# Kernel tuning notes

Hardware: AMD Instinct MI355X
Metric: run time of the kernel (lower is better)

## Reference

```python
import jax, jax.numpy as jnp
import numpy as np

N = 100000      # nodes
E = 1600000     # edges (avg degree 16)
IN, HID, OUT = 64, 64, 32
R = 8           # relations


def setup_inputs() -> dict:
    key = jax.random.key(0)
    ks = jax.random.split(key, 8)
    s = jnp.float32(0.05)  # weight init scale
    return {
        "feat": jax.random.normal(ks[0], (N, IN), dtype=jnp.float32),
        "src": jax.random.randint(ks[1], (E,), 0, N),
        "dst": jax.random.randint(ks[2], (E,), 0, N),
        "etypes": jax.random.randint(ks[3], (E,), 0, R),
        "W1": jax.random.normal(ks[4], (R, IN, HID), dtype=jnp.float32) * s,
        "Wself1": jax.random.normal(ks[5], (IN, HID), dtype=jnp.float32) * s,
        "b1": jnp.zeros((HID,), jnp.float32),
        "W2": jax.random.normal(ks[6], (R, HID, OUT), dtype=jnp.float32) * s,
        "Wself2": jax.random.normal(ks[7], (HID, OUT), dtype=jnp.float32) * s,
        "b2": jnp.zeros((OUT,), jnp.float32),
    }


def _rel_graph_conv(h, src, dst, etypes, W, Wself, b):
    """RelGraphConv with sum aggregation, self-loop and bias.

    h: [N, din], W: [R, din, dout], Wself: [din, dout], b: [dout].
    """
    n = h.shape[0]
    # Transform all nodes by all relation weights once: [R, N, dout].
    hW = jnp.einsum('nd,rdo->rno', h, W)
    # Per-edge message: relation-specific transform of the source node.
    msg = hW[etypes, src]                                    # [E, dout]
    # Scatter-add messages to destination nodes.
    agg = jax.ops.segment_sum(msg, dst, num_segments=n)      # [N, dout]
    return agg + h @ Wself + b


def reference(feat, src, dst, etypes, W1, Wself1, b1, W2, Wself2, b2):
    x = jax.nn.relu(_rel_graph_conv(feat, src, dst, etypes, W1, Wself1, b1))
    return _rel_graph_conv(x, src, dst, etypes, W2, Wself2, b2)
```

## Files before the change

kernel.cpp:

```cpp
#include <hip/hip_runtime.h>
#include <hip/hip_bf16.h>

typedef __attribute__((ext_vector_type(8))) short short8;
typedef __attribute__((ext_vector_type(4))) float f32x4;

__device__ __forceinline__ unsigned short f2bf(float v) {
    __hip_bfloat16 h = __float2bfloat16(v);
    return *reinterpret_cast<unsigned short*>(&h);
}
__device__ __forceinline__ float bf2f(unsigned short u) {
    union { unsigned int i; float f; } x;
    x.i = (unsigned int)u << 16;
    return x.f;
}
__device__ __forceinline__ void acc4(float& s0, float& s1, float& s2, float& s3, uint2 v) {
    s0 += bf2f((unsigned short)(v.x & 0xffff));
    s1 += bf2f((unsigned short)(v.x >> 16));
    s2 += bf2f((unsigned short)(v.y & 0xffff));
    s3 += bf2f((unsigned short)(v.y >> 16));
}

__device__ __forceinline__ void lds_barrier() {
    asm volatile("s_waitcnt lgkmcnt(0)" ::: "memory");
    __builtin_amdgcn_s_barrier();
    asm volatile("" ::: "memory");
}

constexpr int MAXB  = 2048;
constexpr int MAXPB = 1792;

template<int H>
__global__ __launch_bounds__(256) void transpose_w(
    const float* __restrict__ W, const float* __restrict__ Wself,
    unsigned short* __restrict__ Wt, int R)
{
    int i = blockIdx.x * 256 + threadIdx.x;
    int total = (R + 1) * H * 64;
    if (i >= total) return;
    int d = i & 63;
    int hh = i >> 6;
    int r = hh / H, h = hh % H;
    float v = (r < R) ? W[((size_t)r * 64 + d) * H + h]
                      : Wself[(size_t)d * H + h];
    Wt[i] = f2bf(v);
}

template<int H, int RT, bool ABF, bool SBF>
__global__ __launch_bounds__(512) void gemm_rel_mfma(
    const void* __restrict__ Av, const unsigned short* __restrict__ Wt,
    const float* __restrict__ bias,
    unsigned short* __restrict__ C, void* __restrict__ Cselfv,
    int N, int Rrt, int relu)
{
    constexpr int AS = 72;
    constexpr int CPB = (H == 64) ? 72 : 40;
    __shared__ unsigned short As[64 * AS];
    alignas(16) __shared__ float Csf[2][64 * 36];
    const int R = RT ? RT : Rrt;
    const int tid = threadIdx.x;
    const int n0 = blockIdx.x * 64;

    if constexpr (ABF) {
        const unsigned short* A = (const unsigned short*)Av;
        int n = tid >> 3, d8 = (tid & 7) * 8;
        int gn = n0 + n;
        short8 u = {};
        if (gn < N) u = *(const short8*)&A[(size_t)gn * 64 + d8];
        if (relu) {
            #pragma unroll
            for (int j = 0; j < 8; ++j) {
                unsigned short x = (unsigned short)u[j];
                u[j] = (short)((x & 0x8000) ? 0 : x);
            }
        }
        *(short8*)&As[n * AS + d8] = u;
    } else {
        const float* A = (const float*)Av;
        #pragma unroll
        for (int i = 0; i < 2; ++i) {
            int lin = tid + i * 512;
            int n = lin >> 4;
            int d4 = (lin & 15) * 4;
            int gn = n0 + n;
            float4 v = make_float4(0.f, 0.f, 0.f, 0.f);
            if (gn < N) v = *(const float4*)&A[(size_t)gn * 64 + d4];
            if (relu) {
                v.x = fmaxf(v.x, 0.f); v.y = fmaxf(v.y, 0.f);
                v.z = fmaxf(v.z, 0.f); v.w = fmaxf(v.w, 0.f);
            }
            ushort4 u;
            u.x = f2bf(v.x); u.y = f2bf(v.y); u.z = f2bf(v.z); u.w = f2bf(v.w);
            *(ushort4*)&As[n * AS + d4] = u;
        }
    }

    const int w = tid >> 6, lane = tid & 63;
    const int m = lane & 15, quad = lane >> 4;
    const int wt = w & 3;
    const int half = w >> 2;

    lds_barrier();

    short8 afrag[2];
    afrag[0] = *(const short8*)&As[(wt * 16 + m) * AS + 0 * 32 + quad * 8];
    afrag[1] = *(const short8*)&As[(wt * 16 + m) * AS + 1 * 32 + quad * 8];

    constexpr int NT = H / 32;

    auto wptr = [&](int r, int nt, int kc) {
        int colbase = half * (H / 2) + nt * 16;
        return (const short8*)&Wt[((size_t)(r * H + colbase + m)) * 64 + kc * 32 + quad * 8];
    };

    short8 wf0[NT][2], wf1[NT][2];
    #pragma unroll
    for (int nt = 0; nt < NT; ++nt) { wf0[nt][0] = *wptr(0, nt, 0); wf0[nt][1] = *wptr(0, nt, 1); }
    #pragma unroll
    for (int nt = 0; nt < NT; ++nt) { wf1[nt][0] = *wptr(1, nt, 0); wf1[nt][1] = *wptr(1, nt, 1); }

    #pragma unroll
    for (int r = 0; r <= R; ++r) {
        short8 wn[NT][2];
        if (r + 2 <= R) {
            #pragma unroll
            for (int nt = 0; nt < NT; ++nt) {
                wn[nt][0] = *wptr(r + 2, nt, 0);
                wn[nt][1] = *wptr(r + 2, nt, 1);
            }
        }

        f32x4 acc[NT];
        #pragma unroll
        for (int nt = 0; nt < NT; ++nt) {
            acc[nt] = (f32x4){0.f, 0.f, 0.f, 0.f};
            acc[nt] = __builtin_amdgcn_mfma_f32_16x16x32_bf16(wf0[nt][0], afrag[0], acc[nt], 0, 0, 0);
            acc[nt] = __builtin_amdgcn_mfma_f32_16x16x32_bf16(wf0[nt][1], afrag[1], acc[nt], 0, 0, 0);
        }

        unsigned short* Cb = (unsigned short*)Csf[r & 1];
        float* Cf = Csf[r & 1];
        if (r < R) {
            #pragma unroll
            for (int nt = 0; nt < NT; ++nt) {
                int col = half * (H / 2) + nt * 16 + quad * 4;
                ushort4 u;
                u.x = f2bf(acc[nt][0]); u.y = f2bf(acc[nt][1]);
                u.z = f2bf(acc[nt][2]); u.w = f2bf(acc[nt][3]);
                *(ushort4*)&Cb[(wt * 16 + m) * CPB + col] = u;
            }
        } else if constexpr (SBF) {
            #pragma unroll
            for (int nt = 0; nt < NT; ++nt) {
                int col = half * (H / 2) + nt * 16 + quad * 4;
                const float4 bv = *(const float4*)&bias[col];
                ushort4 u;
                u.x = f2bf(acc[nt][0] + bv.x); u.y = f2bf(acc[nt][1] + bv.y);
                u.z = f2bf(acc[nt][2] + bv.z); u.w = f2bf(acc[nt][3] + bv.w);
                *(ushort4*)&Cb[(wt * 16 + m) * CPB + col] = u;
            }
        } else {
            #pragma unroll
            for (int nt = 0; nt < NT; ++nt) {
                int col = half * (H / 2) + nt * 16 + quad * 4;
                const float4 bv = *(const float4*)&bias[col];
                float4 o = make_float4(acc[nt][0] + bv.x, acc[nt][1] + bv.y,
                                       acc[nt][2] + bv.z, acc[nt][3] + bv.w);
                *(float4*)&Cf[(wt * 16 + m) * 36 + col] = o;
            }
        }

        lds_barrier();

        if (r < R) {
            if (H == 64) {
                int rw = tid >> 3, ch = tid & 7;
                int gn = n0 + rw;
                if (gn < N) {
                    uint4 v = *(const uint4*)&Cb[rw * CPB + ch * 8];
                    *(uint4*)&C[((size_t)r * N + gn) * H + ch * 8] = v;
                }
            } else {
                if (tid < 256) {
                    int rw = tid >> 2, ch = tid & 3;
                    int gn = n0 + rw;
                    if (gn < N) {
                        uint4 v = *(const uint4*)&Cb[rw * CPB + ch * 8];
                        *(uint4*)&C[((size_t)r * N + gn) * H + ch * 8] = v;
                    }
                }
            }
        } else if constexpr (SBF) {
            unsigned short* Cs = (unsigned short*)Cselfv;
            int rw = tid >> 3, ch = tid & 7;
            int gn = n0 + rw;
            if (gn < N) {
                uint4 v = *(const uint4*)&Cb[rw * CPB + ch * 8];
                *(uint4*)&Cs[(size_t)gn * H + ch * 8] = v;
            }
        } else {
            float* outf = (float*)Cselfv;
            int rw = tid >> 3, ch = tid & 7;
            int gn = n0 + rw;
            if (gn < N) {
                float4 v = *(const float4*)&Cf[rw * 36 + ch * 4];
                *(float4*)&outf[(size_t)gn * 32 + ch * 4] = v;
            }
        }

        #pragma unroll
        for (int nt = 0; nt < NT; ++nt) {
            wf0[nt][0] = wf1[nt][0]; wf0[nt][1] = wf1[nt][1];
            wf1[nt][0] = wn[nt][0];  wf1[nt][1] = wn[nt][1];
        }
    }
}

__global__ __launch_bounds__(256) void zero_int(int* __restrict__ p, int n) {
    int i = blockIdx.x * 256 + threadIdx.x;
    if (i < n) p[i] = 0;
}

__global__ __launch_bounds__(256) void partition_pad(
    const int* __restrict__ src, const int* __restrict__ dst,
    const int* __restrict__ et, int* __restrict__ gcnt,
    int* __restrict__ rec, int E, int N, int B, int CH)
{
    __shared__ int cnt[MAXB];
    __shared__ int base[MAXB];
    const int t = threadIdx.x;
    const int e0 = blockIdx.x * CH, e1 = min(E, e0 + CH);

    for (int i = t; i < B; i += 256) cnt[i] = 0;
    __syncthreads();
    for (int e = e0 + t; e < e1; e += 256) atomicAdd(&cnt[dst[e] >> 6], 1);
    __syncthreads();
    for (int i = t; i < B; i += 256) {
        int h = cnt[i];
        base[i] = h ? atomicAdd(&gcnt[i], h) : 0;
        cnt[i] = 0;
    }
    __syncthreads();
    for (int e = e0 + t; e < e1; e += 256) {
        int d = dst[e];
        int b = d >> 6;
        int pos = base[b] + atomicAdd(&cnt[b], 1);
        if (pos < MAXPB)
            rec[(size_t)b * MAXPB + pos] = ((et[e] * N + src[e]) << 6) | (d & 63);
    }
}

__global__ __launch_bounds__(256) void bucket_sort(
    const int* __restrict__ gcnt, const int* __restrict__ rec,
    int* __restrict__ eidx, int* __restrict__ rs, int* __restrict__ re_,
    int N)
{
    __shared__ int hist[64];
    __shared__ int excl[64];
    __shared__ int cur[64];
    const int b = blockIdx.x;
    const int tid = threadIdx.x;
    const int p0 = b * MAXPB;
    const int ne = min(gcnt[b], MAXPB);

    if (tid < 64) hist[tid] = 0;
    __syncthreads();
    for (int p = tid; p < ne; p += 256)
        atomicAdd(&hist[rec[p0 + p] & 63], 1);
    __syncthreads();
    if (tid == 0) {
        int run = 0;
        #pragma unroll
        for (int i = 0; i < 64; ++i) { excl[i] = run; run += hist[i]; }
    }
    __syncthreads();
    if (tid < 64) {
        cur[tid] = excl[tid];
        int n = b * 64 + tid;
        if (n < N) {
            rs[n]  = p0 + excl[tid];
            re_[n] = p0 + excl[tid] + hist[tid];
        }
    }
    __syncthreads();
    for (int p = tid; p < ne; p += 256) {
        int rv = rec[p0 + p];
        int pos = p0 + atomicAdd(&cur[rv & 63], 1);
        eidx[pos] = rv >> 6;
    }
}

__global__ __launch_bounds__(256) void agg_csr64(
    const unsigned int* __restrict__ hw32, const int* __restrict__ rs,
    const int* __restrict__ re_, const int* __restrict__ eidx,
    unsigned int* __restrict__ out32, int N)
{
    const int d = blockIdx.x * 4 + (threadIdx.x >> 6);
    const int lane = threadIdx.x & 63;
    if (d >= N) return;
    const int g = lane >> 4;
    const int c = lane & 15;
    const int p0 = rs[d], p1 = re_[d];
    float s0 = 0.f, s1 = 0.f, s2 = 0.f, s3 = 0.f;
    int p = p0 + g;
    for (; p + 12 < p1; p += 16) {
        uint2 v0 = *(const uint2*)&hw32[(size_t)eidx[p]      * 32 + 2 * c];
        uint2 v1 = *(const uint2*)&hw32[(size_t)eidx[p + 4]  * 32 + 2 * c];
        uint2 v2 = *(const uint2*)&hw32[(size_t)eidx[p + 8]  * 32 + 2 * c];
        uint2 v3 = *(const uint2*)&hw32[(size_t)eidx[p + 12] * 32 + 2 * c];
        acc4(s0, s1, s2, s3, v0);
        acc4(s0, s1, s2, s3, v1);
        acc4(s0, s1, s2, s3, v2);
        acc4(s0, s1, s2, s3, v3);
    }
    for (; p < p1; p += 4) {
        uint2 v = *(const uint2*)&hw32[(size_t)eidx[p] * 32 + 2 * c];
        acc4(s0, s1, s2, s3, v);
    }
    s0 += __shfl_xor(s0, 16, 64); s1 += __shfl_xor(s1, 16, 64);
    s2 += __shfl_xor(s2, 16, 64); s3 += __shfl_xor(s3, 16, 64);
    s0 += __shfl_xor(s0, 32, 64); s1 += __shfl_xor(s1, 32, 64);
    s2 += __shfl_xor(s2, 32, 64); s3 += __shfl_xor(s3, 32, 64);
    if (g == 0) {
        uint2 cur = *(const uint2*)&out32[(size_t)d * 32 + 2 * c];
        float o0 = s0 + bf2f((unsigned short)(cur.x & 0xffff));
        float o1 = s1 + bf2f((unsigned short)(cur.x >> 16));
        float o2 = s2 + bf2f((unsigned short)(cur.y & 0xffff));
        float o3 = s3 + bf2f((unsigned short)(cur.y >> 16));
        uint2 o;
        o.x = (unsigned int)f2bf(o0) | ((unsigned int)f2bf(o1) << 16);
        o.y = (unsigned int)f2bf(o2) | ((unsigned int)f2bf(o3) << 16);
        *(uint2*)&out32[(size_t)d * 32 + 2 * c] = o;
    }
}

__global__ __launch_bounds__(256) void agg_csr32(
    const unsigned int* __restrict__ hw32, const int* __restrict__ rs,
    const int* __restrict__ re_, const int* __restrict__ eidx,
    float* __restrict__ out, int N)
{
    const int d = blockIdx.x * 8 + (threadIdx.x >> 5);
    const int l = threadIdx.x & 31;
    if (d >= N) return;
    const int g = l >> 3;
    const int c = l & 7;
    const int p0 = rs[d], p1 = re_[d];
    float s0 = 0.f, s1 = 0.f, s2 = 0.f, s3 = 0.f;
    int p = p0 + g;
    for (; p + 12 < p1; p += 16) {
        uint2 v0 = *(const uint2*)&hw32[(size_t)eidx[p]      * 16 + 2 * c];
        uint2 v1 = *(const uint2*)&hw32[(size_t)eidx[p + 4]  * 16 + 2 * c];
        uint2 v2 = *(const uint2*)&hw32[(size_t)eidx[p + 8]  * 16 + 2 * c];
        uint2 v3 = *(const uint2*)&hw32[(size_t)eidx[p + 12] * 16 + 2 * c];
        acc4(s0, s1, s2, s3, v0);
        acc4(s0, s1, s2, s3, v1);
        acc4(s0, s1, s2, s3, v2);
        acc4(s0, s1, s2, s3, v3);
    }
    for (; p < p1; p += 4) {
        uint2 v = *(const uint2*)&hw32[(size_t)eidx[p] * 16 + 2 * c];
        acc4(s0, s1, s2, s3, v);
    }
    s0 += __shfl_xor(s0, 8, 64);  s1 += __shfl_xor(s1, 8, 64);
    s2 += __shfl_xor(s2, 8, 64);  s3 += __shfl_xor(s3, 8, 64);
    s0 += __shfl_xor(s0, 16, 64); s1 += __shfl_xor(s1, 16, 64);
    s2 += __shfl_xor(s2, 16, 64); s3 += __shfl_xor(s3, 16, 64);
    if (g == 0) {
        float4 cur = *(const float4*)&out[(size_t)d * 32 + 4 * c];
        float4 o = make_float4(cur.x + s0, cur.y + s1, cur.z + s2, cur.w + s3);
        *(float4*)&out[(size_t)d * 32 + 4 * c] = o;
    }
}

extern "C" void kernel_launch(void* const* d_in, const int* in_sizes, int n_in,
                              void* d_out, int out_size, void* d_ws, size_t ws_size,
                              hipStream_t stream)
{
    const float* feat = (const float*)d_in[0];
    const int*   src  = (const int*)d_in[1];
    const int*   dst  = (const int*)d_in[2];
    const int*   et   = (const int*)d_in[3];
    const float* W1   = (const float*)d_in[4];
    const float* Ws1  = (const float*)d_in[5];
    const float* b1   = (const float*)d_in[6];
    const float* W2   = (const float*)d_in[7];
    const float* Ws2  = (const float*)d_in[8];
    const float* b2   = (const float*)d_in[9];
    float* out = (float*)d_out;

    const int N = in_sizes[0] / 64;
    const int E = in_sizes[1];
    const int R = in_sizes[4] / (64 * 64);
    const int B = (N + 63) / 64;

    unsigned short* hW  = (unsigned short*)d_ws;
    unsigned short* h1  = hW + (size_t)R * N * 64;
    unsigned short* Wt1 = h1 + (size_t)N * 64;
    unsigned short* Wt2 = Wt1 + (size_t)(R + 1) * 64 * 64;
    int*   gcnt  = (int*)(Wt2 + (size_t)(R + 1) * 32 * 64);
    int*   rs    = gcnt + B;
    int*   re_   = rs + N;
    int*   rec   = re_ + N;
    int*   eidx  = rec + (size_t)B * MAXPB;

    const dim3 blk(256);
    const int nblk64 = (N + 63) / 64;
    const int P  = 512;
    const int CH = (E + P - 1) / P;

    transpose_w<64><<<((R + 1) * 64 * 64 + 255) / 256, blk, 0, stream>>>(W1, Ws1, Wt1, R);
    transpose_w<32><<<((R + 1) * 32 * 64 + 255) / 256, blk, 0, stream>>>(W2, Ws2, Wt2, R);

    zero_int<<<(B + 255) / 256, blk, 0, stream>>>(gcnt, B);
    partition_pad<<<P, blk, 0, stream>>>(src, dst, et, gcnt, rec, E, N, B, CH);
    bucket_sort<<<B, blk, 0, stream>>>(gcnt, rec, eidx, rs, re_, N);

    if (R == 8)
        gemm_rel_mfma<64, 8, false, true><<<nblk64, 512, 0, stream>>>(feat, Wt1, b1, hW, h1, N, R, 0);
    else
        gemm_rel_mfma<64, 0, false, true><<<nblk64, 512, 0, stream>>>(feat, Wt1, b1, hW, h1, N, R, 0);
    agg_csr64<<<dim3((N + 3) / 4), blk, 0, stream>>>((const unsigned int*)hW, rs, re_, eidx,
                                                     (unsigned int*)h1, N);

    if (R == 8)
        gemm_rel_mfma<32, 8, true, false><<<nblk64, 512, 0, stream>>>(h1, Wt2, b2, hW, out, N, R, 1);
    else
        gemm_rel_mfma<32, 0, true, false><<<nblk64, 512, 0, stream>>>(h1, Wt2, b2, hW, out, N, R, 1);
    agg_csr32<<<dim3((N + 7) / 8), blk, 0, stream>>>((const unsigned int*)hW, rs, re_, eidx, out, N);
}
```

Measured before the change: 337.2 us.

## Fuse edge partition with layer-1 GEMM in one launch and merge weight transposes

```diff
diff --git a/kernel.cpp b/kernel.cpp
--- a/kernel.cpp
+++ b/kernel.cpp
@@ -28,37 +28,73 @@
 
 constexpr int MAXB  = 2048;
 constexpr int MAXPB = 1792;
-
-template<int H>
-__global__ __launch_bounds__(256) void transpose_w(
-    const float* __restrict__ W, const float* __restrict__ Wself,
-    unsigned short* __restrict__ Wt, int R)
+constexpr int SMEM  = 64 * 72 * 2 + 2 * 64 * 36 * 4;
+
+__global__ __launch_bounds__(256) void transpose_both(
+    const float* __restrict__ W1, const float* __restrict__ Ws1,
+    const float* __restrict__ W2, const float* __restrict__ Ws2,
+    unsigned short* __restrict__ Wt1, unsigned short* __restrict__ Wt2, int R)
 {
     int i = blockIdx.x * 256 + threadIdx.x;
-    int total = (R + 1) * H * 64;
-    if (i >= total) return;
-    int d = i & 63;
-    int hh = i >> 6;
-    int r = hh / H, h = hh % H;
-    float v = (r < R) ? W[((size_t)r * 64 + d) * H + h]
-                      : Wself[(size_t)d * H + h];
-    Wt[i] = f2bf(v);
+    int t1 = (R + 1) * 64 * 64;
+    int t2 = (R + 1) * 32 * 64;
+    if (i < t1) {
+        int d = i & 63, hh = i >> 6;
+        int r = hh >> 6, h = hh & 63;
+        float v = (r < R) ? W1[((size_t)r * 64 + d) * 64 + h] : Ws1[(size_t)d * 64 + h];
+        Wt1[i] = f2bf(v);
+    } else if (i < t1 + t2) {
+        int j = i - t1;
+        int d = j & 63, hh = j >> 6;
+        int r = hh >> 5, h = hh & 31;
+        float v = (r < R) ? W2[((size_t)r * 64 + d) * 32 + h] : Ws2[(size_t)d * 32 + h];
+        Wt2[j] = f2bf(v);
+    }
+}
+
+__device__ __forceinline__ void partition_body(
+    char* smem, const int* __restrict__ src, const int* __restrict__ dst,
+    const int* __restrict__ et, int* __restrict__ gcnt,
+    int* __restrict__ rec, int E, int N, int B, int CH, int bidx)
+{
+    int* cnt  = (int*)smem;
+    int* base = (int*)(smem + sizeof(int) * MAXB);
+    const int t = threadIdx.x;
+    const int e0 = bidx * CH, e1 = min(E, e0 + CH);
+
+    for (int i = t; i < B; i += 512) cnt[i] = 0;
+    __syncthreads();
+    for (int e = e0 + t; e < e1; e += 512) atomicAdd(&cnt[dst[e] >> 6], 1);
+    __syncthreads();
+    for (int i = t; i < B; i += 512) {
+        int h = cnt[i];
+        base[i] = h ? atomicAdd(&gcnt[i], h) : 0;
+        cnt[i] = 0;
+    }
+    __syncthreads();
+    for (int e = e0 + t; e < e1; e += 512) {
+        int d = dst[e];
+        int b = d >> 6;
+        int pos = base[b] + atomicAdd(&cnt[b], 1);
+        if (pos < MAXPB)
+            rec[(size_t)b * MAXPB + pos] = ((et[e] * N + src[e]) << 6) | (d & 63);
+    }
 }
 
 template<int H, int RT, bool ABF, bool SBF>
-__global__ __launch_bounds__(512) void gemm_rel_mfma(
-    const void* __restrict__ Av, const unsigned short* __restrict__ Wt,
+__device__ __forceinline__ void gemm_body(
+    char* smem, const void* __restrict__ Av, const unsigned short* __restrict__ Wt,
     const float* __restrict__ bias,
     unsigned short* __restrict__ C, void* __restrict__ Cselfv,
-    int N, int Rrt, int relu)
+    int N, int Rrt, int relu, int bidx)
 {
     constexpr int AS = 72;
     constexpr int CPB = (H == 64) ? 72 : 40;
-    __shared__ unsigned short As[64 * AS];
-    alignas(16) __shared__ float Csf[2][64 * 36];
+    unsigned short* As = (unsigned short*)smem;
+    float* CsfBase = (float*)(smem + 64 * AS * 2);
     const int R = RT ? RT : Rrt;
     const int tid = threadIdx.x;
-    const int n0 = blockIdx.x * 64;
+    const int n0 = bidx * 64;
 
     if constexpr (ABF) {
         const unsigned short* A = (const unsigned short*)Av;
@@ -137,8 +173,8 @@
             acc[nt] = __builtin_amdgcn_mfma_f32_16x16x32_bf16(wf0[nt][1], afrag[1], acc[nt], 0, 0, 0);
         }
 
-        unsigned short* Cb = (unsigned short*)Csf[r & 1];
-        float* Cf = Csf[r & 1];
+        float* Cf = CsfBase + (r & 1) * (64 * 36);
+        unsigned short* Cb = (unsigned short*)Cf;
         if (r < R) {
             #pragma unroll
             for (int nt = 0; nt < NT; ++nt) {
@@ -215,38 +251,33 @@
     }
 }
 
-__global__ __launch_bounds__(256) void zero_int(int* __restrict__ p, int n) {
-    int i = blockIdx.x * 256 + threadIdx.x;
-    if (i < n) p[i] = 0;
-}
-
-__global__ __launch_bounds__(256) void partition_pad(
+template<int RT>
+__global__ __launch_bounds__(512) void mega64(
+    const float* __restrict__ feat, const unsigned short* __restrict__ Wt1,
+    const float* __restrict__ b1, unsigned short* __restrict__ hW,
+    unsigned short* __restrict__ h1,
     const int* __restrict__ src, const int* __restrict__ dst,
-    const int* __restrict__ et, int* __restrict__ gcnt,
-    int* __restrict__ rec, int E, int N, int B, int CH)
-{
-    __shared__ int cnt[MAXB];
-    __shared__ int base[MAXB];
-    const int t = threadIdx.x;
-    const int e0 = blockIdx.x * CH, e1 = min(E, e0 + CH);
-
-    for (int i = t; i < B; i += 256) cnt[i] = 0;
-    __syncthreads();
-    for (int e = e0 + t; e < e1; e += 256) atomicAdd(&cnt[dst[e] >> 6], 1);
-    __syncthreads();
-    for (int i = t; i < B; i += 256) {
-        int h = cnt[i];
-        base[i] = h ? atomicAdd(&gcnt[i], h) : 0;
-        cnt[i] = 0;
-    }
-    __syncthreads();
-    for (int e = e0 + t; e < e1; e += 256) {
-        int d = dst[e];
-        int b = d >> 6;
-        int pos = base[b] + atomicAdd(&cnt[b], 1);
-        if (pos < MAXPB)
-            rec[(size_t)b * MAXPB + pos] = ((et[e] * N + src[e]) << 6) | (d & 63);
-    }
+    const int* __restrict__ et, int* __restrict__ gcnt, int* __restrict__ rec,
+    int E, int N, int B, int CH, int P, int R)
+{
+    __shared__ alignas(16) char smem[SMEM];
+    if ((int)blockIdx.x < P) {
+        partition_body(smem, src, dst, et, gcnt, rec, E, N, B, CH, blockIdx.x);
+    } else {
+        gemm_body<64, RT, false, true>(smem, feat, Wt1, b1, hW, h1, N, R, 0,
+                                       blockIdx.x - P);
+    }
+}
+
+template<int H, int RT, bool ABF, bool SBF>
+__global__ __launch_bounds__(512) void gemm_rel_mfma(
+    const void* __restrict__ Av, const unsigned short* __restrict__ Wt,
+    const float* __restrict__ bias,
+    unsigned short* __restrict__ C, void* __restrict__ Cselfv,
+    int N, int Rrt, int relu)
+{
+    __shared__ alignas(16) char smem[SMEM];
+    gemm_body<H, RT, ABF, SBF>(smem, Av, Wt, bias, C, Cselfv, N, Rrt, relu, blockIdx.x);
 }
 
 __global__ __launch_bounds__(256) void bucket_sort(
@@ -407,17 +438,23 @@
     const int P  = 512;
     const int CH = (E + P - 1) / P;
 
-    transpose_w<64><<<((R + 1) * 64 * 64 + 255) / 256, blk, 0, stream>>>(W1, Ws1, Wt1, R);
-    transpose_w<32><<<((R + 1) * 32 * 64 + 255) / 256, blk, 0, stream>>>(W2, Ws2, Wt2, R);
-
-    zero_int<<<(B + 255) / 256, blk, 0, stream>>>(gcnt, B);
-    partition_pad<<<P, blk, 0, stream>>>(src, dst, et, gcnt, rec, E, N, B, CH);
+    hipMemsetAsync(gcnt, 0, (size_t)B * sizeof(int), stream);
+    {
+        int total = (R + 1) * 96 * 64;
+        transpose_both<<<(total + 255) / 256, blk, 0, stream>>>(W1, Ws1, W2, Ws2, Wt1, Wt2, R);
+    }
+
+    if (R == 8)
+        mega64<8><<<P + nblk64, 512, 0, stream>>>(feat, Wt1, b1, hW, h1,
+                                                  src, dst, et, gcnt, rec,
+                                                  E, N, B, CH, P, R);
+    else
+        mega64<0><<<P + nblk64, 512, 0, stream>>>(feat, Wt1, b1, hW, h1,
+                                                  src, dst, et, gcnt, rec,
+                                                  E, N, B, CH, P, R);
+
     bucket_sort<<<B, blk, 0, stream>>>(gcnt, rec, eidx, rs, re_, N);
 
-    if (R == 8)
-        gemm_rel_mfma<64, 8, false, true><<<nblk64, 512, 0, stream>>>(feat, Wt1, b1, hW, h1, N, R, 0);
-    else
-        gemm_rel_mfma<64, 0, false, true><<<nblk64, 512, 0, stream>>>(feat, Wt1, b1, hW, h1, N, R, 0);
     agg_csr64<<<dim3((N + 3) / 4), blk, 0, stream>>>((const unsigned int*)hW, rs, re_, eidx,
                                                      (unsigned int*)h1, N);
 
```

Measured after the change: 319.8 us. -5.2%, faster.
